# Optimization experiments

Hardware: AMD Instinct MI355X
Metric: run time of the kernel (lower is better)

## Reference

```python
import jax, jax.numpy as jnp
import numpy as np

B, T, C = 4, 2048, 1024
H = 16
D = C // H  # 64


def setup_inputs() -> dict:
    key = jax.random.key(0)
    ks = jax.random.split(key, 5)
    scale = 0.02
    x = jax.random.normal(ks[0], (B, T, C), dtype=jnp.float32)
    # Linear weights stored in [in, out] layout (equivalent to torch W.T)
    W_qkv = jax.random.normal(ks[1], (C, 3 * C), dtype=jnp.float32) * scale
    b_qkv = jax.random.normal(ks[2], (3 * C,), dtype=jnp.float32) * scale
    W_out = jax.random.normal(ks[3], (C, C), dtype=jnp.float32) * scale
    b_out = jax.random.normal(ks[4], (C,), dtype=jnp.float32) * scale
    return {"x": x, "W_qkv": W_qkv, "b_qkv": b_qkv, "W_out": W_out, "b_out": b_out}


def reference(x, W_qkv, b_qkv, W_out, b_out):
    Bx, Tx, Cx = x.shape
    qkv = x @ W_qkv + b_qkv                      # [B,T,3C]
    qkv = qkv.reshape(Bx, Tx, 3, H, D)
    q = jnp.transpose(qkv[:, :, 0], (0, 2, 1, 3))  # [B,H,T,D]
    k = jnp.transpose(qkv[:, :, 1], (0, 2, 1, 3))
    v = jnp.transpose(qkv[:, :, 2], (0, 2, 1, 3))
    scores = jnp.einsum('bhqd,bhkd->bhqk', q, k) / jnp.sqrt(jnp.float32(D))
    causal = jnp.tril(jnp.ones((Tx, Tx), dtype=bool))  # keep lower triangle
    scores = jnp.where(causal, scores, jnp.float32(-jnp.inf))
    w = jax.nn.softmax(scores, axis=-1)           # dropout p=0.0 (eval)
    out = jnp.einsum('bhqk,bhkd->bhqd', w, v)     # [B,H,T,D]
    out = jnp.transpose(out, (0, 2, 1, 3)).reshape(Bx, Tx, Cx)
    return out @ W_out + b_out
```

## Files before the change

kernel.cpp:

```cpp
#include <hip/hip_runtime.h>

typedef _Float16 f16;
typedef _Float16 f16x4 __attribute__((ext_vector_type(4)));
typedef _Float16 f16x8 __attribute__((ext_vector_type(8)));
typedef float    f32x4 __attribute__((ext_vector_type(4)));

#define B_ 4
#define T_ 2048
#define C_ 1024
#define H_ 16
#define D_ 64

#if __has_builtin(__builtin_amdgcn_exp2f)
#define FAST_EXP(x) __builtin_amdgcn_exp2f(x)
#define QSCALE (0.125f * 1.44269504f)
#define POFF 8.0f
#else
#define FAST_EXP(x) __expf(x)
#define QSCALE 0.125f
#define POFF 5.5452f
#endif

__device__ __forceinline__ void gload_lds16(const f16* g, f16* l) {
  __builtin_amdgcn_global_load_lds(
      (const __attribute__((address_space(1))) unsigned int*)g,
      (__attribute__((address_space(3))) unsigned int*)l, 16, 0, 0);
}

__global__ void cvt_kernel(const float* __restrict__ in, f16* __restrict__ out, int n4) {
  int i = blockIdx.x * blockDim.x + threadIdx.x;
  int stride = gridDim.x * blockDim.x;
  for (; i < n4; i += stride) {
    float4 v = ((const float4*)in)[i];
    f16x4 h = { (f16)v.x, (f16)v.y, (f16)v.z, (f16)v.w };
    ((f16x4*)out)[i] = h;
  }
}

__global__ void transpose2_kernel(const float* __restrict__ Wqkv, f16* __restrict__ WqkvT,
                                  const float* __restrict__ Wout, f16* __restrict__ WoutT) {
  __shared__ f16 tile[32][33];
  const int K = 1024;
  int bx = blockIdx.x, by = blockIdx.y;
  const float* W; f16* Wt; int N;
  if (bx < 96) { W = Wqkv; Wt = WqkvT; N = 3072; }
  else         { W = Wout; Wt = WoutT; N = 1024; bx -= 96; }
  int tx = threadIdx.x & 31, ty = threadIdx.x >> 5;
  #pragma unroll
  for (int i = ty; i < 32; i += 8)
    tile[i][tx] = (f16)W[(size_t)(by * 32 + i) * N + bx * 32 + tx];
  __syncthreads();
  #pragma unroll
  for (int i = ty; i < 32; i += 8)
    Wt[(size_t)(bx * 32 + i) * K + by * 32 + tx] = tile[tx][i];
}

__global__ __launch_bounds__(256, 2)
void gemmW_kernel(const f16* __restrict__ A, const f16* __restrict__ Bt,
                  const float* __restrict__ bias,
                  f16* __restrict__ q, f16* __restrict__ kk, f16* __restrict__ vt) {
  const int K = 1024, N = 3072;
  __shared__ __align__(16) f16 As[3][256 * 32];
  __shared__ __align__(16) f16 Bs[3][128 * 32];
  const int nbn = N >> 7;
  const int bid = blockIdx.x;
  const int bm = bid / nbn, bn = bid % nbn;
  const int m0 = bm << 8, n0 = bn << 7;
  const int tid = threadIdx.x;
  const int lane = tid & 63, wid = tid >> 6;
  const int wm = wid >> 1, wn = wid & 1;

  f32x4 acc[8][4] = {};

  const int srow = lane >> 2;
  const int scol = (((lane & 3) ^ ((lane >> 2) & 3)) << 3);
  const f16* Abase = A + (size_t)(m0 + srow) * K + scol;
  const f16* Bbase = Bt + (size_t)(n0 + srow) * K + scol;

  auto stage = [&](int buf, int kt) {
    #pragma unroll
    for (int c = 0; c < 4; ++c) {
      const int cA = (wid << 2) + c;
      gload_lds16(Abase + (size_t)cA * 16 * K + kt * 32, &As[buf][cA * 512]);
    }
    #pragma unroll
    for (int c = 0; c < 2; ++c) {
      const int cB = (wid << 1) + c;
      gload_lds16(Bbase + (size_t)cB * 16 * K + kt * 32, &Bs[buf][cB * 512]);
    }
  };

  const int g = lane >> 4;
  const int rr = lane & 15;
  const int swz = (g ^ (rr & 3)) << 4;

  auto compute = [&](int buf) {
    f16x8 bf[4];
    #pragma unroll
    for (int t = 0; t < 4; ++t)
      bf[t] = *(const f16x8*)((const char*)&Bs[buf][0] + (wn * 64 + t * 16 + rr) * 64 + swz);
    #pragma unroll
    for (int mh = 0; mh < 2; ++mh) {
      f16x8 af[4];
      #pragma unroll
      for (int t = 0; t < 4; ++t)
        af[t] = *(const f16x8*)((const char*)&As[buf][0]
                 + (wm * 128 + mh * 64 + t * 16 + rr) * 64 + swz);
      __builtin_amdgcn_s_setprio(1);
      #pragma unroll
      for (int i = 0; i < 4; ++i)
        #pragma unroll
        for (int j = 0; j < 4; ++j)
          acc[mh * 4 + i][j] =
              __builtin_amdgcn_mfma_f32_16x16x32_f16(af[i], bf[j], acc[mh * 4 + i][j], 0, 0, 0);
      __builtin_amdgcn_s_setprio(0);
    }
  };

  const int nk = K >> 5;
  int bcur = 0, bnext = 1, bnn = 2;
  stage(0, 0);
  stage(1, 1);
  asm volatile("s_waitcnt vmcnt(6)" ::: "memory");
  __builtin_amdgcn_s_barrier();
  __builtin_amdgcn_sched_barrier(0);
  for (int t = 0; t < nk; ++t) {
    if (t + 2 < nk) stage(bnn, t + 2);
    compute(bcur);
    if (t + 1 < nk) {
      if (t + 2 < nk) asm volatile("s_waitcnt vmcnt(6)" ::: "memory");
      else            asm volatile("s_waitcnt vmcnt(0)" ::: "memory");
      __builtin_amdgcn_s_barrier();
      __builtin_amdgcn_sched_barrier(0);
    }
    const int tmp = bcur; bcur = bnext; bnext = bnn; bnn = tmp;
  }

  const int col = lane & 15;
  const int row4 = (lane >> 4) << 2;
  #pragma unroll
  for (int mi = 0; mi < 8; ++mi) {
    #pragma unroll
    for (int j = 0; j < 4; ++j) {
      const int n = n0 + wn * 64 + j * 16 + col;
      const float bn_ = bias[n];
      const int cc = n & 1023;
      const int h = cc >> 6, d = cc & 63;
      const int which = n >> 10;
      #pragma unroll
      for (int r = 0; r < 4; ++r) {
        const int m = m0 + wm * 128 + mi * 16 + row4 + r;
        const float v = acc[mi][j][r] + bn_;
        const int b = m >> 11, t = m & 2047;
        const size_t bh = (size_t)b * 16 + h;
        const f16 hv = (f16)v;
        if (which == 0)      q [(bh * T_ + t) * D_ + d] = hv;
        else if (which == 1) kk[(bh * T_ + t) * D_ + d] = hv;
        else                 vt[(bh * D_ + d) * T_ + t] = hv;
      }
    }
  }
}

__global__ __launch_bounds__(256, 3)
void gemm_kernel(const f16* __restrict__ A, const f16* __restrict__ Bt,
                 const float* __restrict__ bias, float* __restrict__ outF,
                 int M, int N, int K) {
  __shared__ __align__(16) f16 As[3][128 * 32];
  __shared__ __align__(16) f16 Bs[3][128 * 32];
  const int nbn = N >> 7;
  const int bid = blockIdx.x;
  const int bm = bid / nbn, bn = bid % nbn;
  const int m0 = bm << 7, n0 = bn << 7;
  const int tid = threadIdx.x;
  const int lane = tid & 63, wid = tid >> 6;
  const int wr = wid >> 1, wc = wid & 1;

  f32x4 acc[4][4] = {};

  const int srow = lane >> 2;
  const int scol = (((lane & 3) ^ ((lane >> 2) & 3)) << 3);
  const f16* Abase = A + (size_t)(m0 + srow) * K + scol;
  const f16* Bbase = Bt + (size_t)(n0 + srow) * K + scol;

  auto stage = [&](int buf, int kt) {
    const int c0 = wid * 2;
    #pragma unroll
    for (int c = c0; c < c0 + 2; ++c) {
      gload_lds16(Abase + (size_t)c * 16 * K + kt * 32, &As[buf][c * 512]);
      gload_lds16(Bbase + (size_t)c * 16 * K + kt * 32, &Bs[buf][c * 512]);
    }
  };

  const int g = lane >> 4;
  const int rr = lane & 15;
  const int swz = (g ^ (rr & 3)) << 4;

  auto compute = [&](int buf) {
    f16x8 af[4], bf[4];
    #pragma unroll
    for (int t = 0; t < 4; ++t) {
      af[t] = *(const f16x8*)((const char*)&As[buf][0] + (wr * 64 + t * 16 + rr) * 64 + swz);
      bf[t] = *(const f16x8*)((const char*)&Bs[buf][0] + (wc * 64 + t * 16 + rr) * 64 + swz);
    }
    __builtin_amdgcn_s_setprio(1);
    #pragma unroll
    for (int i = 0; i < 4; ++i)
      #pragma unroll
      for (int j = 0; j < 4; ++j)
        acc[i][j] = __builtin_amdgcn_mfma_f32_16x16x32_f16(af[i], bf[j], acc[i][j], 0, 0, 0);
    __builtin_amdgcn_s_setprio(0);
  };

  const int nk = K >> 5;
  int bcur = 0, bnext = 1, bnn = 2;
  stage(0, 0);
  stage(1, 1);
  asm volatile("s_waitcnt vmcnt(4)" ::: "memory");
  __builtin_amdgcn_s_barrier();
  __builtin_amdgcn_sched_barrier(0);
  for (int t = 0; t < nk; ++t) {
    if (t + 2 < nk) stage(bnn, t + 2);
    compute(bcur);
    if (t + 1 < nk) {
      if (t + 2 < nk) asm volatile("s_waitcnt vmcnt(4)" ::: "memory");
      else            asm volatile("s_waitcnt vmcnt(0)" ::: "memory");
      __builtin_amdgcn_s_barrier();
      __builtin_amdgcn_sched_barrier(0);
    }
    const int tmp = bcur; bcur = bnext; bnext = bnn; bnn = tmp;
  }

  const int col = lane & 15;
  const int row4 = (lane >> 4) << 2;
  #pragma unroll
  for (int i = 0; i < 4; ++i) {
    #pragma unroll
    for (int j = 0; j < 4; ++j) {
      const int n = n0 + wc * 64 + j * 16 + col;
      const float bn_ = bias[n];
      #pragma unroll
      for (int r = 0; r < 4; ++r) {
        const int m = m0 + wr * 64 + i * 16 + row4 + r;
        outF[(size_t)m * N + n] = acc[i][j][r] + bn_;
      }
    }
  }
}

__global__ __launch_bounds__(256, 3)
void attn_kernel(const f16* __restrict__ Q, const f16* __restrict__ Kg,
                 const f16* __restrict__ Vt, f16* __restrict__ Aout) {
  __shared__ __align__(16) f16 Ks[2][64 * 64];
  __shared__ __align__(16) f16 Vs[2][64 * 64];
  __shared__ __align__(16) f16 Pt[4][32 * 64];

  const int bid = blockIdx.x;
  const int wgid = (bid & 7) * 64 + (bid >> 3);
  const int bh = wgid >> 3;
  const int pr = wgid & 7;
  const int lane = threadIdx.x & 63, w = threadIdx.x >> 6;
  const int col = lane & 15;
  const int g = lane >> 4;
  const int ko = g << 3;

  const f16* Qp = Q + (size_t)bh * T_ * D_;
  const f16* Kp = Kg + (size_t)bh * T_ * D_;
  const f16* Vp = Vt + (size_t)bh * D_ * T_;

  const int sr = lane >> 3;
  const int sc = ((lane & 7) ^ (sr & 7)) << 3;

  auto stage = [&](int buf, int kb) {
    #pragma unroll
    for (int c2 = 0; c2 < 2; ++c2) {
      const int c = (w << 1) + c2;
      gload_lds16(Kp + (size_t)(kb + (c << 3) + sr) * D_ + sc, &Ks[buf][c * 512]);
      gload_lds16(Vp + (size_t)((c << 3) + sr) * T_ + kb + sc, &Vs[buf][c * 512]);
    }
  };
  auto ldsK = [&](int buf, int krow, int d0) -> f16x8 {
    const int off = krow * 128 + ((d0 << 1) ^ ((krow & 7) << 4));
    return *(const f16x8*)((const char*)&Ks[buf][0] + off);
  };
  auto ldsV = [&](int buf, int drow, int k0) -> f16x8 {
    const int off = drow * 128 + ((k0 << 1) ^ ((drow & 7) << 4));
    return *(const f16x8*)((const char*)&Vs[buf][0] + off);
  };

  char* PtW = (char*)&Pt[w][0];
  const int b = bh >> 4, hd = bh & 15;

  #pragma unroll 1
  for (int tt = 0; tt < 2; ++tt) {
    const int ti = tt ? (15 - pr) : pr;
    const int qrow0 = (ti << 7) + (w << 5);
    const int nkt = (ti << 1) + 2;

    const f16 qsc = (f16)QSCALE;
    f16x8 qf[2][2];
    #pragma unroll
    for (int h = 0; h < 2; ++h)
      #pragma unroll
      for (int s = 0; s < 2; ++s) {
        f16x8 t = *(const f16x8*)&Qp[(size_t)(qrow0 + h * 16 + col) * D_ + s * 32 + ko];
        #pragma unroll
        for (int e = 0; e < 8; ++e) t[e] = t[e] * qsc;
        qf[h][s] = t;
      }

    f32x4 o[2][4] = {};
    float lp[2] = {0.f, 0.f};

    auto COMPUTE = [&](int buf, int kb) {
      f32x4 sc2[2][4] = {};
      __builtin_amdgcn_s_setprio(1);
      #pragma unroll
      for (int s = 0; s < 2; ++s)
        #pragma unroll
        for (int mt = 0; mt < 4; ++mt) {
          f16x8 kf = ldsK(buf, mt * 16 + col, s * 32 + ko);
          sc2[0][mt] = __builtin_amdgcn_mfma_f32_16x16x32_f16(kf, qf[0][s], sc2[0][mt], 0, 0, 0);
          sc2[1][mt] = __builtin_amdgcn_mfma_f32_16x16x32_f16(kf, qf[1][s], sc2[1][mt], 0, 0, 0);
        }
      __builtin_amdgcn_s_setprio(0);

      if (kb + 63 > qrow0) {
        #pragma unroll
        for (int mt = 0; mt < 4; ++mt)
          #pragma unroll
          for (int r = 0; r < 4; ++r) {
            const int kv = kb + mt * 16 + (g << 2) + r;
            if (kv > qrow0 + col)      sc2[0][mt][r] = -1e30f;
            if (kv > qrow0 + 16 + col) sc2[1][mt][r] = -1e30f;
          }
      }

      #pragma unroll
      for (int h = 0; h < 2; ++h) {
        #pragma unroll
        for (int mt = 0; mt < 4; ++mt) {
          f16x4 ph;
          #pragma unroll
          for (int r = 0; r < 4; ++r) {
            const float p = FAST_EXP(sc2[h][mt][r] - POFF);
            lp[h] += p;
            ph[r] = (f16)p;
          }
          *(f16x4*)(PtW + (h * 16 + col) * 128 + (((mt << 5) + (g << 3)) ^ ((col & 7) << 4))) = ph;
        }
      }

      __builtin_amdgcn_s_setprio(1);
      #pragma unroll
      for (int s = 0; s < 2; ++s) {
        const int pcb = ((s << 6) + (g << 4)) ^ ((col & 7) << 4);
        f16x8 pb0 = *(const f16x8*)(PtW + col * 128 + pcb);
        f16x8 pb1 = *(const f16x8*)(PtW + (16 + col) * 128 + pcb);
        #pragma unroll
        for (int mt = 0; mt < 4; ++mt) {
          f16x8 vf = ldsV(buf, mt * 16 + col, s * 32 + ko);
          o[0][mt] = __builtin_amdgcn_mfma_f32_16x16x32_f16(vf, pb0, o[0][mt], 0, 0, 0);
          o[1][mt] = __builtin_amdgcn_mfma_f32_16x16x32_f16(vf, pb1, o[1][mt], 0, 0, 0);
        }
      }
      __builtin_amdgcn_s_setprio(0);
    };

    stage(0, 0);
    asm volatile("s_waitcnt vmcnt(0)" ::: "memory");
    __builtin_amdgcn_s_barrier();
    __builtin_amdgcn_sched_barrier(0);

    #pragma unroll 1
    for (int kt = 0; kt < nkt; ++kt) {
      if (kt + 1 < nkt) stage((kt + 1) & 1, (kt + 1) << 6);
      COMPUTE(kt & 1, kt << 6);

      __builtin_amdgcn_sched_barrier(0);
      asm volatile("s_waitcnt vmcnt(0)" ::: "memory");
      __builtin_amdgcn_s_barrier();
      __builtin_amdgcn_sched_barrier(0);
    }

    #pragma unroll
    for (int h = 0; h < 2; ++h) {
      float l = lp[h];
      l += __shfl_xor(l, 16, 64);
      l += __shfl_xor(l, 32, 64);
      const float inv = 1.0f / l;
      const int t = qrow0 + h * 16 + col;
      const size_t rowoff = ((size_t)b * T_ + t) * C_ + (size_t)hd * D_;
      #pragma unroll
      for (int mt = 0; mt < 4; ++mt) {
        f16x4 ov;
        #pragma unroll
        for (int r = 0; r < 4; ++r) ov[r] = (f16)(o[h][mt][r] * inv);
        *(f16x4*)&Aout[rowoff + mt * 16 + (g << 2)] = ov;
      }
    }
    __builtin_amdgcn_s_barrier();
  }
}

extern "C" void kernel_launch(void* const* d_in, const int* in_sizes, int n_in,
                              void* d_out, int out_size, void* d_ws, size_t ws_size,
                              hipStream_t stream) {
  const float* x    = (const float*)d_in[0];
  const float* Wqkv = (const float*)d_in[1];
  const float* bqkv = (const float*)d_in[2];
  const float* Wout = (const float*)d_in[3];
  const float* bout = (const float*)d_in[4];
  float* out = (float*)d_out;

  char* ws = (char*)d_ws;
  f16* xb     = (f16*)ws;
  f16* Wqkv_t = (f16*)(ws + (16u << 20));
  f16* Wout_t = (f16*)(ws + (22u << 20));
  f16* Qb     = (f16*)(ws + (24u << 20));
  f16* Kb     = (f16*)(ws + (40u << 20));
  f16* Vtb    = (f16*)(ws + (56u << 20));

  cvt_kernel<<<2048, 256, 0, stream>>>(x, xb, (B_ * T_ * C_) / 4);
  dim3 gt(128, 32);
  transpose2_kernel<<<gt, 256, 0, stream>>>(Wqkv, Wqkv_t, Wout, Wout_t);

  gemmW_kernel<<<768, 256, 0, stream>>>(xb, Wqkv_t, bqkv, Qb, Kb, Vtb);
  attn_kernel<<<512, 256, 0, stream>>>(Qb, Kb, Vtb, xb );
  gemm_kernel<<<512, 256, 0, stream>>>(xb, Wout_t, bout, out, 8192, 1024, 1024);
}
```

Baseline: 206.7 us.

## Fuse fp32-to-fp16 input conversion into QKV GEMM and split attention tiles

The separate cvt kernel is removed, and the QKV GEMM now loads fp32 x through registers, converts it to fp16 and writes it to LDS, using a smaller 128x128 tile with higher occupancy. The attention kernel launches one workgroup per query tile (1024 blocks) instead of pairing light and heavy tiles within one block. It also skips fully masked KV tiles per wave and keeps row sums as vectors. This saves a full pass over x and a launch, at the cost of register-staged A loads (no direct-to-LDS), doubled A/B re-reads across the smaller tiles, and the load balancing that the paired attention tiles used to provide.

```diff
diff --git a/kernel.cpp b/kernel.cpp
--- a/kernel.cpp
+++ b/kernel.cpp
@@ -27,16 +27,6 @@
       (__attribute__((address_space(3))) unsigned int*)l, 16, 0, 0);
 }
 
-__global__ void cvt_kernel(const float* __restrict__ in, f16* __restrict__ out, int n4) {
-  int i = blockIdx.x * blockDim.x + threadIdx.x;
-  int stride = gridDim.x * blockDim.x;
-  for (; i < n4; i += stride) {
-    float4 v = ((const float4*)in)[i];
-    f16x4 h = { (f16)v.x, (f16)v.y, (f16)v.z, (f16)v.w };
-    ((f16x4*)out)[i] = h;
-  }
-}
-
 __global__ void transpose2_kernel(const float* __restrict__ Wqkv, f16* __restrict__ WqkvT,
                                   const float* __restrict__ Wout, f16* __restrict__ WoutT) {
   __shared__ f16 tile[32][33];
@@ -55,39 +45,54 @@
     Wt[(size_t)(bx * 32 + i) * K + by * 32 + tx] = tile[tx][i];
 }
 
-__global__ __launch_bounds__(256, 2)
-void gemmW_kernel(const f16* __restrict__ A, const f16* __restrict__ Bt,
+__global__ __launch_bounds__(256, 3)
+void gemmX_kernel(const float* __restrict__ X, const f16* __restrict__ Bt,
                   const float* __restrict__ bias,
                   f16* __restrict__ q, f16* __restrict__ kk, f16* __restrict__ vt) {
   const int K = 1024, N = 3072;
-  __shared__ __align__(16) f16 As[3][256 * 32];
+  __shared__ __align__(16) f16 As[3][128 * 32];
   __shared__ __align__(16) f16 Bs[3][128 * 32];
   const int nbn = N >> 7;
   const int bid = blockIdx.x;
   const int bm = bid / nbn, bn = bid % nbn;
-  const int m0 = bm << 8, n0 = bn << 7;
+  const int m0 = bm << 7, n0 = bn << 7;
   const int tid = threadIdx.x;
   const int lane = tid & 63, wid = tid >> 6;
-  const int wm = wid >> 1, wn = wid & 1;
-
-  f32x4 acc[8][4] = {};
+  const int wr = wid >> 1, wc = wid & 1;
+
+  f32x4 acc[4][4] = {};
 
   const int srow = lane >> 2;
   const int scol = (((lane & 3) ^ ((lane >> 2) & 3)) << 3);
-  const f16* Abase = A + (size_t)(m0 + srow) * K + scol;
+  const float* Xbase = X + (size_t)(m0 + srow) * K + scol;
   const f16* Bbase = Bt + (size_t)(n0 + srow) * K + scol;
 
-  auto stage = [&](int buf, int kt) {
-    #pragma unroll
-    for (int c = 0; c < 4; ++c) {
-      const int cA = (wid << 2) + c;
-      gload_lds16(Abase + (size_t)cA * 16 * K + kt * 32, &As[buf][cA * 512]);
-    }
-    #pragma unroll
-    for (int c = 0; c < 2; ++c) {
-      const int cB = (wid << 1) + c;
-      gload_lds16(Bbase + (size_t)cB * 16 * K + kt * 32, &Bs[buf][cB * 512]);
-    }
+  auto stageB = [&](int buf, int kt) {
+    const int c0 = wid * 2;
+    #pragma unroll
+    for (int c = c0; c < c0 + 2; ++c)
+      gload_lds16(Bbase + (size_t)c * 16 * K + kt * 32, &Bs[buf][c * 512]);
+  };
+
+  float4 ar0a, ar0b, ar1a, ar1b;
+  auto loadA = [&](int kt) {
+    const int c0 = wid * 2;
+    const float* p0 = Xbase + (size_t)c0 * 16 * K + kt * 32;
+    const float* p1 = Xbase + (size_t)(c0 + 1) * 16 * K + kt * 32;
+    ar0a = *(const float4*)(p0);
+    ar0b = *(const float4*)(p0 + 4);
+    ar1a = *(const float4*)(p1);
+    ar1b = *(const float4*)(p1 + 4);
+  };
+  auto writeA = [&](int buf) {
+    const int c0 = wid * 2;
+    f16x8 h0, h1;
+    h0[0]=(f16)ar0a.x; h0[1]=(f16)ar0a.y; h0[2]=(f16)ar0a.z; h0[3]=(f16)ar0a.w;
+    h0[4]=(f16)ar0b.x; h0[5]=(f16)ar0b.y; h0[6]=(f16)ar0b.z; h0[7]=(f16)ar0b.w;
+    h1[0]=(f16)ar1a.x; h1[1]=(f16)ar1a.y; h1[2]=(f16)ar1a.z; h1[3]=(f16)ar1a.w;
+    h1[4]=(f16)ar1b.x; h1[5]=(f16)ar1b.y; h1[6]=(f16)ar1b.z; h1[7]=(f16)ar1b.w;
+    *(f16x8*)&As[buf][c0 * 512 + lane * 8] = h0;
+    *(f16x8*)&As[buf][(c0 + 1) * 512 + lane * 8] = h1;
   };
 
   const int g = lane >> 4;
@@ -95,41 +100,40 @@
   const int swz = (g ^ (rr & 3)) << 4;
 
   auto compute = [&](int buf) {
-    f16x8 bf[4];
-    #pragma unroll
-    for (int t = 0; t < 4; ++t)
-      bf[t] = *(const f16x8*)((const char*)&Bs[buf][0] + (wn * 64 + t * 16 + rr) * 64 + swz);
-    #pragma unroll
-    for (int mh = 0; mh < 2; ++mh) {
-      f16x8 af[4];
-      #pragma unroll
-      for (int t = 0; t < 4; ++t)
-        af[t] = *(const f16x8*)((const char*)&As[buf][0]
-                 + (wm * 128 + mh * 64 + t * 16 + rr) * 64 + swz);
-      __builtin_amdgcn_s_setprio(1);
-      #pragma unroll
-      for (int i = 0; i < 4; ++i)
-        #pragma unroll
-        for (int j = 0; j < 4; ++j)
-          acc[mh * 4 + i][j] =
-              __builtin_amdgcn_mfma_f32_16x16x32_f16(af[i], bf[j], acc[mh * 4 + i][j], 0, 0, 0);
-      __builtin_amdgcn_s_setprio(0);
-    }
+    f16x8 af[4], bf[4];
+    #pragma unroll
+    for (int t = 0; t < 4; ++t) {
+      af[t] = *(const f16x8*)((const char*)&As[buf][0] + (wr * 64 + t * 16 + rr) * 64 + swz);
+      bf[t] = *(const f16x8*)((const char*)&Bs[buf][0] + (wc * 64 + t * 16 + rr) * 64 + swz);
+    }
+    __builtin_amdgcn_s_setprio(1);
+    #pragma unroll
+    for (int i = 0; i < 4; ++i)
+      #pragma unroll
+      for (int j = 0; j < 4; ++j)
+        acc[i][j] = __builtin_amdgcn_mfma_f32_16x16x32_f16(af[i], bf[j], acc[i][j], 0, 0, 0);
+    __builtin_amdgcn_s_setprio(0);
   };
 
   const int nk = K >> 5;
   int bcur = 0, bnext = 1, bnn = 2;
-  stage(0, 0);
-  stage(1, 1);
-  asm volatile("s_waitcnt vmcnt(6)" ::: "memory");
+  loadA(0);
+  stageB(0, 0);
+  stageB(1, 1);
+  asm volatile("s_waitcnt vmcnt(2)" ::: "memory");
+  writeA(0);
+  asm volatile("s_waitcnt lgkmcnt(0)" ::: "memory");
   __builtin_amdgcn_s_barrier();
   __builtin_amdgcn_sched_barrier(0);
   for (int t = 0; t < nk; ++t) {
-    if (t + 2 < nk) stage(bnn, t + 2);
+    if (t + 1 < nk) loadA(t + 1);
+    if (t + 2 < nk) stageB(bnn, t + 2);
     compute(bcur);
     if (t + 1 < nk) {
-      if (t + 2 < nk) asm volatile("s_waitcnt vmcnt(6)" ::: "memory");
+      if (t + 2 < nk) asm volatile("s_waitcnt vmcnt(2)" ::: "memory");
       else            asm volatile("s_waitcnt vmcnt(0)" ::: "memory");
+      writeA(bnext);
+      asm volatile("s_waitcnt lgkmcnt(0)" ::: "memory");
       __builtin_amdgcn_s_barrier();
       __builtin_amdgcn_sched_barrier(0);
     }
@@ -139,18 +143,18 @@
   const int col = lane & 15;
   const int row4 = (lane >> 4) << 2;
   #pragma unroll
-  for (int mi = 0; mi < 8; ++mi) {
+  for (int i = 0; i < 4; ++i) {
     #pragma unroll
     for (int j = 0; j < 4; ++j) {
-      const int n = n0 + wn * 64 + j * 16 + col;
+      const int n = n0 + wc * 64 + j * 16 + col;
       const float bn_ = bias[n];
       const int cc = n & 1023;
       const int h = cc >> 6, d = cc & 63;
       const int which = n >> 10;
       #pragma unroll
       for (int r = 0; r < 4; ++r) {
-        const int m = m0 + wm * 128 + mi * 16 + row4 + r;
-        const float v = acc[mi][j][r] + bn_;
+        const int m = m0 + wr * 64 + i * 16 + row4 + r;
+        const float v = acc[i][j][r] + bn_;
         const int b = m >> 11, t = m & 2047;
         const size_t bh = (size_t)b * 16 + h;
         const f16 hv = (f16)v;
@@ -256,9 +260,9 @@
   __shared__ __align__(16) f16 Pt[4][32 * 64];
 
   const int bid = blockIdx.x;
-  const int wgid = (bid & 7) * 64 + (bid >> 3);
-  const int bh = wgid >> 3;
-  const int pr = wgid & 7;
+  const int xcd = bid & 7, k = bid >> 3;
+  const int bh = (xcd << 3) + (k & 7);
+  const int ti = 15 - (k >> 3);
   const int lane = threadIdx.x & 63, w = threadIdx.x >> 6;
   const int col = lane & 15;
   const int g = lane >> 4;
@@ -291,115 +295,110 @@
   char* PtW = (char*)&Pt[w][0];
   const int b = bh >> 4, hd = bh & 15;
 
+  const int qrow0 = (ti << 7) + (w << 5);
+  const int nkt = (ti << 1) + 2;
+
+  const f16 qsc = (f16)QSCALE;
+  f16x8 qf[2][2];
+  #pragma unroll
+  for (int h = 0; h < 2; ++h)
+    #pragma unroll
+    for (int s = 0; s < 2; ++s) {
+      f16x8 t = *(const f16x8*)&Qp[(size_t)(qrow0 + h * 16 + col) * D_ + s * 32 + ko];
+      #pragma unroll
+      for (int e = 0; e < 8; ++e) t[e] = t[e] * qsc;
+      qf[h][s] = t;
+    }
+
+  f32x4 o[2][4] = {};
+  f32x4 lpv[2] = {};
+
+  auto COMPUTE = [&](int buf, int kb) {
+    f32x4 sc2[2][4] = {};
+    __builtin_amdgcn_s_setprio(1);
+    #pragma unroll
+    for (int s = 0; s < 2; ++s)
+      #pragma unroll
+      for (int mt = 0; mt < 4; ++mt) {
+        f16x8 kf = ldsK(buf, mt * 16 + col, s * 32 + ko);
+        sc2[0][mt] = __builtin_amdgcn_mfma_f32_16x16x32_f16(kf, qf[0][s], sc2[0][mt], 0, 0, 0);
+        sc2[1][mt] = __builtin_amdgcn_mfma_f32_16x16x32_f16(kf, qf[1][s], sc2[1][mt], 0, 0, 0);
+      }
+    __builtin_amdgcn_s_setprio(0);
+
+    if (kb + 63 > qrow0) {
+      #pragma unroll
+      for (int mt = 0; mt < 4; ++mt)
+        #pragma unroll
+        for (int r = 0; r < 4; ++r) {
+          const int kv = kb + mt * 16 + (g << 2) + r;
+          if (kv > qrow0 + col)      sc2[0][mt][r] = -1e30f;
+          if (kv > qrow0 + 16 + col) sc2[1][mt][r] = -1e30f;
+        }
+    }
+
+    #pragma unroll
+    for (int h = 0; h < 2; ++h) {
+      #pragma unroll
+      for (int mt = 0; mt < 4; ++mt) {
+        f16x4 ph;
+        #pragma unroll
+        for (int r = 0; r < 4; ++r) {
+          const float p = FAST_EXP(sc2[h][mt][r] - POFF);
+          lpv[h][r] += p;
+          ph[r] = (f16)p;
+        }
+        *(f16x4*)(PtW + (h * 16 + col) * 128 + (((mt << 5) + (g << 3)) ^ ((col & 7) << 4))) = ph;
+      }
+    }
+
+    __builtin_amdgcn_s_setprio(1);
+    #pragma unroll
+    for (int s = 0; s < 2; ++s) {
+      const int pcb = ((s << 6) + (g << 4)) ^ ((col & 7) << 4);
+      f16x8 pb0 = *(const f16x8*)(PtW + col * 128 + pcb);
+      f16x8 pb1 = *(const f16x8*)(PtW + (16 + col) * 128 + pcb);
+      #pragma unroll
+      for (int mt = 0; mt < 4; ++mt) {
+        f16x8 vf = ldsV(buf, mt * 16 + col, s * 32 + ko);
+        o[0][mt] = __builtin_amdgcn_mfma_f32_16x16x32_f16(vf, pb0, o[0][mt], 0, 0, 0);
+        o[1][mt] = __builtin_amdgcn_mfma_f32_16x16x32_f16(vf, pb1, o[1][mt], 0, 0, 0);
+      }
+    }
+    __builtin_amdgcn_s_setprio(0);
+  };
+
+  stage(0, 0);
+  asm volatile("s_waitcnt vmcnt(0)" ::: "memory");
+  __builtin_amdgcn_s_barrier();
+  __builtin_amdgcn_sched_barrier(0);
+
   #pragma unroll 1
-  for (int tt = 0; tt < 2; ++tt) {
-    const int ti = tt ? (15 - pr) : pr;
-    const int qrow0 = (ti << 7) + (w << 5);
-    const int nkt = (ti << 1) + 2;
-
-    const f16 qsc = (f16)QSCALE;
-    f16x8 qf[2][2];
-    #pragma unroll
-    for (int h = 0; h < 2; ++h)
-      #pragma unroll
-      for (int s = 0; s < 2; ++s) {
-        f16x8 t = *(const f16x8*)&Qp[(size_t)(qrow0 + h * 16 + col) * D_ + s * 32 + ko];
-        #pragma unroll
-        for (int e = 0; e < 8; ++e) t[e] = t[e] * qsc;
-        qf[h][s] = t;
-      }
-
-    f32x4 o[2][4] = {};
-    float lp[2] = {0.f, 0.f};
-
-    auto COMPUTE = [&](int buf, int kb) {
-      f32x4 sc2[2][4] = {};
-      __builtin_amdgcn_s_setprio(1);
-      #pragma unroll
-      for (int s = 0; s < 2; ++s)
-        #pragma unroll
-        for (int mt = 0; mt < 4; ++mt) {
-          f16x8 kf = ldsK(buf, mt * 16 + col, s * 32 + ko);
-          sc2[0][mt] = __builtin_amdgcn_mfma_f32_16x16x32_f16(kf, qf[0][s], sc2[0][mt], 0, 0, 0);
-          sc2[1][mt] = __builtin_amdgcn_mfma_f32_16x16x32_f16(kf, qf[1][s], sc2[1][mt], 0, 0, 0);
-        }
-      __builtin_amdgcn_s_setprio(0);
-
-      if (kb + 63 > qrow0) {
-        #pragma unroll
-        for (int mt = 0; mt < 4; ++mt)
-          #pragma unroll
-          for (int r = 0; r < 4; ++r) {
-            const int kv = kb + mt * 16 + (g << 2) + r;
-            if (kv > qrow0 + col)      sc2[0][mt][r] = -1e30f;
-            if (kv > qrow0 + 16 + col) sc2[1][mt][r] = -1e30f;
-          }
-      }
-
-      #pragma unroll
-      for (int h = 0; h < 2; ++h) {
-        #pragma unroll
-        for (int mt = 0; mt < 4; ++mt) {
-          f16x4 ph;
-          #pragma unroll
-          for (int r = 0; r < 4; ++r) {
-            const float p = FAST_EXP(sc2[h][mt][r] - POFF);
-            lp[h] += p;
-            ph[r] = (f16)p;
-          }
-          *(f16x4*)(PtW + (h * 16 + col) * 128 + (((mt << 5) + (g << 3)) ^ ((col & 7) << 4))) = ph;
-        }
-      }
-
-      __builtin_amdgcn_s_setprio(1);
-      #pragma unroll
-      for (int s = 0; s < 2; ++s) {
-        const int pcb = ((s << 6) + (g << 4)) ^ ((col & 7) << 4);
-        f16x8 pb0 = *(const f16x8*)(PtW + col * 128 + pcb);
-        f16x8 pb1 = *(const f16x8*)(PtW + (16 + col) * 128 + pcb);
-        #pragma unroll
-        for (int mt = 0; mt < 4; ++mt) {
-          f16x8 vf = ldsV(buf, mt * 16 + col, s * 32 + ko);
-          o[0][mt] = __builtin_amdgcn_mfma_f32_16x16x32_f16(vf, pb0, o[0][mt], 0, 0, 0);
-          o[1][mt] = __builtin_amdgcn_mfma_f32_16x16x32_f16(vf, pb1, o[1][mt], 0, 0, 0);
-        }
-      }
-      __builtin_amdgcn_s_setprio(0);
-    };
-
-    stage(0, 0);
+  for (int kt = 0; kt < nkt; ++kt) {
+    if (kt + 1 < nkt) stage((kt + 1) & 1, (kt + 1) << 6);
+    if ((kt << 6) <= qrow0 + 31) COMPUTE(kt & 1, kt << 6);
+
+    __builtin_amdgcn_sched_barrier(0);
     asm volatile("s_waitcnt vmcnt(0)" ::: "memory");
     __builtin_amdgcn_s_barrier();
     __builtin_amdgcn_sched_barrier(0);
-
-    #pragma unroll 1
-    for (int kt = 0; kt < nkt; ++kt) {
-      if (kt + 1 < nkt) stage((kt + 1) & 1, (kt + 1) << 6);
-      COMPUTE(kt & 1, kt << 6);
-
-      __builtin_amdgcn_sched_barrier(0);
-      asm volatile("s_waitcnt vmcnt(0)" ::: "memory");
-      __builtin_amdgcn_s_barrier();
-      __builtin_amdgcn_sched_barrier(0);
-    }
-
-    #pragma unroll
-    for (int h = 0; h < 2; ++h) {
-      float l = lp[h];
-      l += __shfl_xor(l, 16, 64);
-      l += __shfl_xor(l, 32, 64);
-      const float inv = 1.0f / l;
-      const int t = qrow0 + h * 16 + col;
-      const size_t rowoff = ((size_t)b * T_ + t) * C_ + (size_t)hd * D_;
-      #pragma unroll
-      for (int mt = 0; mt < 4; ++mt) {
-        f16x4 ov;
-        #pragma unroll
-        for (int r = 0; r < 4; ++r) ov[r] = (f16)(o[h][mt][r] * inv);
-        *(f16x4*)&Aout[rowoff + mt * 16 + (g << 2)] = ov;
-      }
-    }
-    __builtin_amdgcn_s_barrier();
+  }
+
+  #pragma unroll
+  for (int h = 0; h < 2; ++h) {
+    float l = lpv[h][0] + lpv[h][1] + lpv[h][2] + lpv[h][3];
+    l += __shfl_xor(l, 16, 64);
+    l += __shfl_xor(l, 32, 64);
+    const float inv = 1.0f / l;
+    const int t = qrow0 + h * 16 + col;
+    const size_t rowoff = ((size_t)b * T_ + t) * C_ + (size_t)hd * D_;
+    #pragma unroll
+    for (int mt = 0; mt < 4; ++mt) {
+      f16x4 ov;
+      #pragma unroll
+      for (int r = 0; r < 4; ++r) ov[r] = (f16)(o[h][mt][r] * inv);
+      *(f16x4*)&Aout[rowoff + mt * 16 + (g << 2)] = ov;
+    }
   }
 }
 
@@ -421,11 +420,10 @@
   f16* Kb     = (f16*)(ws + (40u << 20));
   f16* Vtb    = (f16*)(ws + (56u << 20));
 
-  cvt_kernel<<<2048, 256, 0, stream>>>(x, xb, (B_ * T_ * C_) / 4);
   dim3 gt(128, 32);
   transpose2_kernel<<<gt, 256, 0, stream>>>(Wqkv, Wqkv_t, Wout, Wout_t);
 
-  gemmW_kernel<<<768, 256, 0, stream>>>(xb, Wqkv_t, bqkv, Qb, Kb, Vtb);
-  attn_kernel<<<512, 256, 0, stream>>>(Qb, Kb, Vtb, xb );
-  gemm_kernel<<<512, 256, 0, stream>>>(xb, Wout_t, bout, out, 8192, 1024, 1024);
-}
+  gemmX_kernel<<<64 * 24, 256, 0, stream>>>(x, Wqkv_t, bqkv, Qb, Kb, Vtb);
+  attn_kernel<<<1024, 256, 0, stream>>>(Qb, Kb, Vtb, xb );
+  gemm_kernel<<<64 * 8, 256, 0, stream>>>(xb, Wout_t, bout, out, 8192, 1024, 1024);
+}
```

Result: faster. 190.5 us (-7.9%).
